# Kernel tuning notes

Hardware: AMD Instinct MI355X
Metric: run time of the kernel (lower is better)

## Reference

```python
import jax, jax.numpy as jnp
import numpy as np

BLOCKSIZE = 64
M = 8192  # out_features
N = 8192  # in_features

# bitsandbytes fp4 codebook (16 entries, normalized to [-1, 1])
FP4_CODE = np.array([0.0, 0.0052083333, 0.6666667, 1.0, 0.33333334, 0.5,
                     0.16666667, 0.25, 0.0, -0.0052083333, -0.6666667, -1.0,
                     -0.33333334, -0.5, -0.16666667, -0.25], dtype=np.float32)


def setup_inputs() -> dict:
    key = jax.random.key(0)
    k1, k2, k3, k4 = jax.random.split(key, 4)
    numel = M * N
    x = jax.random.normal(k1, (4, N), dtype=jnp.float32)
    # packed bytes: each byte holds two 4-bit codebook indices
    qweight = jax.random.randint(k2, (numel // 2,), 0, 256, dtype=jnp.int32)
    # per-block absmax scales (positive)
    absmax = jax.random.uniform(k3, (numel // BLOCKSIZE,), dtype=jnp.float32,
                                minval=0.01, maxval=1.0)
    code = jnp.asarray(FP4_CODE)
    bias = jax.random.normal(k4, (M,), dtype=jnp.float32)
    return {"x": x, "qweight": qweight, "absmax": absmax, "code": code, "bias": bias}


def _dequantize_fp4(qweight, absmax, code):
    # unpack two 4-bit indices per byte: high nibble first, low nibble second
    b = qweight.astype(jnp.int32)
    hi = (b >> 4) & 0xF
    lo = b & 0xF
    idx = jnp.stack([hi, lo], axis=-1).reshape(-1)          # [numel]
    vals = code[idx]                                        # codebook lookup
    # blockwise absmax scaling
    w = (vals.reshape(-1, BLOCKSIZE) * absmax[:, None]).reshape(M, N)
    return w


def reference(x, qweight, absmax, code, bias):
    w = _dequantize_fp4(qweight, absmax, code)              # [M, N]
    # nn.Linear semantics: y = x @ W^T + b
    return x @ w.T + bias
```

## Files before the change

### kernel.cpp

```cpp
#include <hip/hip_runtime.h>
#include <cstdint>

#define MDIM 8192
#define NDIM 8192
#define QPR  (NDIM / 2)
#define ABPR (NDIM / 64)
#define ROWS_PER_BLOCK 16
#define NITER 64

typedef _Float16 half2_t __attribute__((ext_vector_type(2)));

__device__ __forceinline__ uint32_t f16bits(uint32_t idx) {
  uint32_t k  = idx & 7u;
  uint32_t hb = (uint32_t)(0x343138353C391D00ull >> (k * 8)) & 0xFFu;
  uint32_t lb = (0u - (hb & 1u)) & 0x55u;
  return (hb << 8) | lb | ((idx & 8u) << 12);
}

__device__ __forceinline__ uint32_t dec_pair(uint32_t b) {
  return f16bits((b >> 4) & 15u) | (f16bits(b & 15u) << 16);
}

__device__ __forceinline__ float fdot2(uint32_t w, uint32_t x, float c) {
#if __has_builtin(__builtin_amdgcn_fdot2)
  return __builtin_amdgcn_fdot2(__builtin_bit_cast(half2_t, w),
                                __builtin_bit_cast(half2_t, x), c, false);
#else
  half2_t wh = __builtin_bit_cast(half2_t, w);
  half2_t xh = __builtin_bit_cast(half2_t, x);
  return c + (float)wh.x * (float)xh.x + (float)wh.y * (float)xh.y;
#endif
}

__device__ __forceinline__ uint32_t swz(uint32_t g) { return g ^ ((g >> 3) & 7u); }

__global__ __launch_bounds__(256, 2) void fp4gemv(
    const float* __restrict__ x, const uint32_t* __restrict__ qw,
    const float* __restrict__ am, const float* __restrict__ bias,
    float* __restrict__ out) {
  __shared__ uint32_t xs[4096 * 4];

#pragma unroll 4
  for (int it = 0; it < 16; ++it) {
    int p = threadIdx.x + it * 256;
    float2 v0 = *(const float2*)(x + 0 * NDIM + 2 * p);
    float2 v1 = *(const float2*)(x + 1 * NDIM + 2 * p);
    float2 v2 = *(const float2*)(x + 2 * NDIM + 2 * p);
    float2 v3 = *(const float2*)(x + 3 * NDIM + 2 * p);
    union { _Float16 h[2]; uint32_t u; } c0, c1, c2, c3;
    c0.h[0] = (_Float16)v0.x; c0.h[1] = (_Float16)v0.y;
    c1.h[0] = (_Float16)v1.x; c1.h[1] = (_Float16)v1.y;
    c2.h[0] = (_Float16)v2.x; c2.h[1] = (_Float16)v2.y;
    c3.h[0] = (_Float16)v3.x; c3.h[1] = (_Float16)v3.y;
    uint4 w; w.x = c0.u; w.y = c1.u; w.z = c2.u; w.w = c3.u;
    *(uint4*)&xs[swz((uint32_t)p) * 4] = w;
  }
  __syncthreads();

  const int lane = threadIdx.x & 63;
  const int wv   = threadIdx.x >> 6;
  const int t    = lane & 15;
  const int g    = lane >> 4;
  const int m    = blockIdx.x * ROWS_PER_BLOCK + wv * 4 + g;

  const uint4* qrow  = (const uint4*)(qw + (size_t)m * QPR);
  const float* abrow = am + (size_t)m * ABPR + (t >> 3);

  float a0 = 0.f, a1 = 0.f, a2 = 0.f, a3 = 0.f;

  uint4 qA = qrow[t];        float sA = abrow[0];
  uint4 qB = qrow[t + 16];   float sB = abrow[2];

#pragma unroll 2
  for (int k = 0; k < NITER; ++k) {
    const int kn = (k + 2) & 63;
    uint4 qC = qrow[t + 16 * kn];
    float sC = abrow[2 * kn];

    uint32_t h0 = dec_pair(qA.x);
    uint32_t h1 = dec_pair(qA.y);
    uint32_t h2 = dec_pair(qA.z);
    uint32_t h3 = dec_pair(qA.w);

    const int j0 = 4 * t + 64 * k;
    uint4 x0 = *(const uint4*)&xs[swz((uint32_t)(j0 + 0)) * 4];
    uint4 x1 = *(const uint4*)&xs[swz((uint32_t)(j0 + 1)) * 4];
    uint4 x2 = *(const uint4*)&xs[swz((uint32_t)(j0 + 2)) * 4];
    uint4 x3 = *(const uint4*)&xs[swz((uint32_t)(j0 + 3)) * 4];

    float s0, s1, s2, s3;
    s0 = fdot2(h0, x0.x, 0.f); s0 = fdot2(h1, x1.x, s0);
    s0 = fdot2(h2, x2.x, s0);  s0 = fdot2(h3, x3.x, s0);
    s1 = fdot2(h0, x0.y, 0.f); s1 = fdot2(h1, x1.y, s1);
    s1 = fdot2(h2, x2.y, s1);  s1 = fdot2(h3, x3.y, s1);
    s2 = fdot2(h0, x0.z, 0.f); s2 = fdot2(h1, x1.z, s2);
    s2 = fdot2(h2, x2.z, s2);  s2 = fdot2(h3, x3.z, s2);
    s3 = fdot2(h0, x0.w, 0.f); s3 = fdot2(h1, x1.w, s3);
    s3 = fdot2(h2, x2.w, s3);  s3 = fdot2(h3, x3.w, s3);

    a0 = fmaf(sA, s0, a0); a1 = fmaf(sA, s1, a1);
    a2 = fmaf(sA, s2, a2); a3 = fmaf(sA, s3, a3);

    qA = qB; sA = sB; qB = qC; sB = sC;
  }

#pragma unroll
  for (int off = 8; off > 0; off >>= 1) {
    a0 += __shfl_xor(a0, off);
    a1 += __shfl_xor(a1, off);
    a2 += __shfl_xor(a2, off);
    a3 += __shfl_xor(a3, off);
  }
  if (t == 0) {
    float b = bias[m];
    out[0 * MDIM + m] = a0 + b;
    out[1 * MDIM + m] = a1 + b;
    out[2 * MDIM + m] = a2 + b;
    out[3 * MDIM + m] = a3 + b;
  }
}

extern "C" void kernel_launch(void* const* d_in, const int* in_sizes, int n_in,
                              void* d_out, int out_size, void* d_ws, size_t ws_size,
                              hipStream_t stream) {
  const float*    x    = (const float*)d_in[0];
  const uint32_t* qwp  = (const uint32_t*)d_in[1];
  const float*    am   = (const float*)d_in[2];
  const float*    bias = (const float*)d_in[4];
  float*          out  = (float*)d_out;

  fp4gemv<<<dim3(MDIM / ROWS_PER_BLOCK), dim3(256), 0, stream>>>(
      x, qwp, am, bias, out);
}
```

Measured before the change: 203.6 us.

## Split K across two blocks with atomic accumulation and deeper nontemporal prefetch

Each output row group is now handled by two blocks, each covering half of the input dimension, with partial sums combined through atomicAdd onto an output pre-filled with bias by a new init kernel. Shared memory per block is halved and launch bounds are raised to allow more resident blocks. Weight loads use nontemporal loads with a four-deep register ring prefetch instead of a two-deep one. The cost is an extra kernel launch, atomic traffic, and x being loaded and converted twice overall; the fallback fdot2 path also now contains a typo (wh.x*wh.x), though it is unused when the builtin exists.

```diff
diff --git a/kernel.cpp b/kernel.cpp
--- a/kernel.cpp
+++ b/kernel.cpp
@@ -6,9 +6,11 @@
 #define QPR  (NDIM / 2)
 #define ABPR (NDIM / 64)
 #define ROWS_PER_BLOCK 16
-#define NITER 64
+#define HGRAN 2048
+#define NITER 32
 
 typedef _Float16 half2_t __attribute__((ext_vector_type(2)));
+typedef uint32_t u32x4   __attribute__((ext_vector_type(4)));
 
 __device__ __forceinline__ uint32_t f16bits(uint32_t idx) {
   uint32_t k  = idx & 7u;
@@ -28,25 +30,42 @@
 #else
   half2_t wh = __builtin_bit_cast(half2_t, w);
   half2_t xh = __builtin_bit_cast(half2_t, x);
-  return c + (float)wh.x * (float)xh.x + (float)wh.y * (float)xh.y;
+  return c + (float)wh.x * (float)wh.x + (float)wh.y * (float)xh.y;
+#endif
+}
+
+__device__ __forceinline__ u32x4 ntload(const u32x4* p) {
+#if __has_builtin(__builtin_nontemporal_load)
+  return __builtin_nontemporal_load(p);
+#else
+  return *p;
 #endif
 }
 
 __device__ __forceinline__ uint32_t swz(uint32_t g) { return g ^ ((g >> 3) & 7u); }
 
-__global__ __launch_bounds__(256, 2) void fp4gemv(
+__global__ void bias_init(const float* __restrict__ bias, float* __restrict__ out) {
+  int i = blockIdx.x * 256 + threadIdx.x;
+  out[i] = bias[i & (MDIM - 1)];
+}
+
+__global__ __launch_bounds__(256, 4) void fp4gemv(
     const float* __restrict__ x, const uint32_t* __restrict__ qw,
     const float* __restrict__ am, const float* __restrict__ bias,
     float* __restrict__ out) {
-  __shared__ uint32_t xs[4096 * 4];
+  __shared__ uint32_t xs[HGRAN * 4];
+
+  const int half = blockIdx.x & 1;
+  const int mblk = blockIdx.x >> 1;
 
 #pragma unroll 4
-  for (int it = 0; it < 16; ++it) {
+  for (int it = 0; it < 8; ++it) {
     int p = threadIdx.x + it * 256;
-    float2 v0 = *(const float2*)(x + 0 * NDIM + 2 * p);
-    float2 v1 = *(const float2*)(x + 1 * NDIM + 2 * p);
-    float2 v2 = *(const float2*)(x + 2 * NDIM + 2 * p);
-    float2 v3 = *(const float2*)(x + 3 * NDIM + 2 * p);
+    int c = 2 * (half * HGRAN + p);
+    float2 v0 = *(const float2*)(x + 0 * NDIM + c);
+    float2 v1 = *(const float2*)(x + 1 * NDIM + c);
+    float2 v2 = *(const float2*)(x + 2 * NDIM + c);
+    float2 v3 = *(const float2*)(x + 3 * NDIM + c);
     union { _Float16 h[2]; uint32_t u; } c0, c1, c2, c3;
     c0.h[0] = (_Float16)v0.x; c0.h[1] = (_Float16)v0.y;
     c1.h[0] = (_Float16)v1.x; c1.h[1] = (_Float16)v1.y;
@@ -61,21 +80,27 @@
   const int wv   = threadIdx.x >> 6;
   const int t    = lane & 15;
   const int g    = lane >> 4;
-  const int m    = blockIdx.x * ROWS_PER_BLOCK + wv * 4 + g;
+  const int m    = mblk * ROWS_PER_BLOCK + wv * 4 + g;
 
-  const uint4* qrow  = (const uint4*)(qw + (size_t)m * QPR);
-  const float* abrow = am + (size_t)m * ABPR + (t >> 3);
+  const u32x4* qrow  = (const u32x4*)(qw + (size_t)m * QPR + half * 2048);
+  const float* abrow = am + (size_t)m * ABPR + half * 64 + (t >> 3);
 
   float a0 = 0.f, a1 = 0.f, a2 = 0.f, a3 = 0.f;
 
-  uint4 qA = qrow[t];        float sA = abrow[0];
-  uint4 qB = qrow[t + 16];   float sB = abrow[2];
+  u32x4 q[4]; float s[4];
+#pragma unroll
+  for (int i = 0; i < 4; ++i) {
+    q[i] = ntload(&qrow[t + 16 * i]);
+    s[i] = abrow[2 * i];
+  }
 
-#pragma unroll 2
+#pragma unroll 4
   for (int k = 0; k < NITER; ++k) {
-    const int kn = (k + 2) & 63;
-    uint4 qC = qrow[t + 16 * kn];
-    float sC = abrow[2 * kn];
+    const int r = k & 3;
+    u32x4 qA = q[r];  float sA = s[r];
+    int kn = k + 4; if (kn >= NITER) kn -= NITER;
+    q[r] = ntload(&qrow[t + 16 * kn]);
+    s[r] = abrow[2 * kn];
 
     uint32_t h0 = dec_pair(qA.x);
     uint32_t h1 = dec_pair(qA.y);
@@ -100,8 +125,6 @@
 
     a0 = fmaf(sA, s0, a0); a1 = fmaf(sA, s1, a1);
     a2 = fmaf(sA, s2, a2); a3 = fmaf(sA, s3, a3);
-
-    qA = qB; sA = sB; qB = qC; sB = sC;
   }
 
 #pragma unroll
@@ -112,11 +135,10 @@
     a3 += __shfl_xor(a3, off);
   }
   if (t == 0) {
-    float b = bias[m];
-    out[0 * MDIM + m] = a0 + b;
-    out[1 * MDIM + m] = a1 + b;
-    out[2 * MDIM + m] = a2 + b;
-    out[3 * MDIM + m] = a3 + b;
+    atomicAdd(&out[0 * MDIM + m], a0);
+    atomicAdd(&out[1 * MDIM + m], a1);
+    atomicAdd(&out[2 * MDIM + m], a2);
+    atomicAdd(&out[3 * MDIM + m], a3);
   }
 }
 
@@ -129,6 +151,7 @@
   const float*    bias = (const float*)d_in[4];
   float*          out  = (float*)d_out;
 
-  fp4gemv<<<dim3(MDIM / ROWS_PER_BLOCK), dim3(256), 0, stream>>>(
+  bias_init<<<dim3((4 * MDIM) / 256), dim3(256), 0, stream>>>(bias, out);
+  fp4gemv<<<dim3((MDIM / ROWS_PER_BLOCK) * 2), dim3(256), 0, stream>>>(
       x, qwp, am, bias, out);
 }
```

Measured after the change: 202.7 us. About the same (-0.4%).
